# Kernel optimization log

Measured on AMD Instinct MI355X. Metric: run time of the kernel, lower is better.

## Reference

```python
import jax, jax.numpy as jnp
import numpy as np

EMB = 768
HEADS = 12


def setup_inputs() -> dict:
    key = jax.random.key(0)
    ks = jax.random.split(key, 5)
    B, N, E = 8, 1024, EMB
    x = jax.random.normal(ks[0], (B, N, E), dtype=jnp.float32)
    s = 1.0 / np.sqrt(E)
    W_qkv = jax.random.normal(ks[1], (E, 3 * E), dtype=jnp.float32) * s
    b_qkv = jnp.zeros((3 * E,), dtype=jnp.float32)
    W_fc = jax.random.normal(ks[2], (E, E), dtype=jnp.float32) * s
    b_fc = jnp.zeros((E,), dtype=jnp.float32)
    return {"x": x, "W_qkv": W_qkv, "b_qkv": b_qkv, "W_fc": W_fc, "b_fc": b_fc}


def reference(x, W_qkv, b_qkv, W_fc, b_fc):
    B, N, E = x.shape
    H = HEADS
    D = E // H
    qkv = x @ W_qkv + b_qkv                      # [B, N, 3E]
    q, k, v = jnp.split(qkv, 3, axis=-1)
    # b n (h d) -> b h n d
    def to_heads(t):
        return t.reshape(B, N, H, D).transpose(0, 2, 1, 3)
    q, k, v = to_heads(q), to_heads(k), to_heads(v)
    scale = 1.0 / jnp.sqrt(jnp.float32(E))       # NOTE: scales by sqrt(emb_size), not head dim
    attn = jnp.einsum('bhid,bhjd->bhij', q, k) * scale
    attn = jax.nn.softmax(attn, axis=-1)
    out = jnp.einsum('bhij,bhjd->bhid', attn, v)
    out = out.transpose(0, 2, 1, 3).reshape(B, N, E)  # b h n d -> b n (h d)
    return out @ W_fc + b_fc
```

## Files before the change

### kernel.cpp

```cpp
#include <hip/hip_runtime.h>
#include <hip/hip_bf16.h>


typedef unsigned short u16;
typedef unsigned int u32;
typedef __attribute__((ext_vector_type(8))) short short8;
typedef __attribute__((ext_vector_type(4))) float f32x4;

#define DEV static __device__ __forceinline__

DEV u16 f2bf(float f) {
  union { float f; u32 u; } v; v.f = f;
  return (u16)((v.u + 0x7FFFu + ((v.u >> 16) & 1u)) >> 16);
}

DEV u32 pk2(float lo, float hi) {
  union { __hip_bfloat162 h2; u32 u; } v;
  v.h2.x = __float2bfloat16(lo);
  v.h2.y = __float2bfloat16(hi);
  return v.u;
}

DEV void gload_lds16(const void* g, void* l) {
  __builtin_amdgcn_global_load_lds(
      (const __attribute__((address_space(1))) void*)g,
      (__attribute__((address_space(3))) void*)l, 16, 0, 0);
}

__global__ void cvt_bf16_kernel(const float* __restrict__ in, u16* __restrict__ out, int n8) {
  int idx = blockIdx.x * blockDim.x + threadIdx.x;
  int stride = gridDim.x * blockDim.x;
  for (int i = idx; i < n8; i += stride) {
    float4 a = reinterpret_cast<const float4*>(in)[2 * i];
    float4 b = reinterpret_cast<const float4*>(in)[2 * i + 1];
    uint4 o;
    o.x = f2bf(a.x) | ((u32)f2bf(a.y) << 16);
    o.y = f2bf(a.z) | ((u32)f2bf(a.w) << 16);
    o.z = f2bf(b.x) | ((u32)f2bf(b.y) << 16);
    o.w = f2bf(b.z) | ((u32)f2bf(b.w) << 16);
    reinterpret_cast<uint4*>(out)[i] = o;
  }
}

__global__ void trcvt_kernel(const float* __restrict__ in, u16* __restrict__ out,
                             int K, int Nn) {
  __shared__ u16 tile[64][72];
  int ntiles = Nn >> 6;
  int tk = blockIdx.x / ntiles, tn = blockIdx.x % ntiles;
  int k0 = tk << 6, n0 = tn << 6;
  int t = threadIdx.x;
  int r = t >> 4;
  int c4 = (t & 15) << 2;
#pragma unroll
  for (int ps = 0; ps < 4; ++ps) {
    int k = r + ps * 16;
    float4 v = *reinterpret_cast<const float4*>(&in[(size_t)(k0 + k) * Nn + n0 + c4]);
    tile[c4 + 0][k] = f2bf(v.x);
    tile[c4 + 1][k] = f2bf(v.y);
    tile[c4 + 2][k] = f2bf(v.z);
    tile[c4 + 3][k] = f2bf(v.w);
  }
  __syncthreads();
  int nr = t >> 3;
  int c8 = (t & 7) << 3;
#pragma unroll
  for (int ps = 0; ps < 2; ++ps) {
    int n = nr + ps * 32;
    uint4 v = *reinterpret_cast<const uint4*>(&tile[n][c8]);
    *reinterpret_cast<uint4*>(&out[(size_t)(n0 + n) * K + k0 + c8]) = v;
  }
}

template <int MODE>
__global__ __launch_bounds__(256, 4) void gemm_bt(
    const u16* __restrict__ A, const u16* __restrict__ Bt,
    const float* __restrict__ bias, void* __restrict__ Cout,
    u16* __restrict__ qh, u16* __restrict__ kh, u16* __restrict__ vt,
    int Nn) {
  __shared__ u16 As[2][128 * 32];
  __shared__ u16 Bs[2][128 * 32];
  const int nTn = Nn >> 7;
  const int nwg = gridDim.x;
  int wg = blockIdx.x;
  wg = (wg & 7) * (nwg >> 3) + (wg >> 3);
  const int tm = wg / nTn, tn = wg % nTn;
  const int m0 = tm << 7, n0 = tn << 7;
  const int tid = threadIdx.x;
  const int w = tid >> 6, lane = tid & 63;
  const int g = lane >> 4, p = lane & 15;
  const int wr = w >> 1, wc = w & 1;

  const int srow = lane >> 2;
  const int schunk = (lane & 3) ^ ((srow >> 1) & 3);
  const u16* Asrc = A + (size_t)(m0 + srow) * 768 + schunk * 8;
  const u16* Bsrc = Bt + (size_t)(n0 + srow) * 768 + schunk * 8;
  const int csw = (g ^ ((p >> 1) & 3)) << 3;

  f32x4 acc[4][4] = {};

#define STAGE(kt, sbuf)                                                         \
  do {                                                                          \
    _Pragma("unroll")                                                           \
    for (int i = 0; i < 2; ++i) {                                               \
      int trow = w * 32 + i * 16;                                               \
      gload_lds16(Asrc + (size_t)trow * 768 + (kt) * 32, &As[sbuf][trow * 32]); \
      gload_lds16(Bsrc + (size_t)trow * 768 + (kt) * 32, &Bs[sbuf][trow * 32]); \
    }                                                                           \
  } while (0)

  STAGE(0, 0);
  __syncthreads();

  int buf = 0;
  for (int k = 0; k < 24; ++k) {
    const u16* as = As[buf];
    const u16* bs = Bs[buf];
    short8 af[4], bf[4];
#pragma unroll
    for (int mb = 0; mb < 4; ++mb)
      af[mb] = *reinterpret_cast<const short8*>(&as[(wr * 64 + mb * 16 + p) * 32 + csw]);
#pragma unroll
    for (int nb = 0; nb < 4; ++nb)
      bf[nb] = *reinterpret_cast<const short8*>(&bs[(wc * 64 + nb * 16 + p) * 32 + csw]);
    if (k < 23) STAGE(k + 1, buf ^ 1);
#pragma unroll
    for (int mb = 0; mb < 4; ++mb)
#pragma unroll
      for (int nb = 0; nb < 4; ++nb)
        acc[mb][nb] = __builtin_amdgcn_mfma_f32_16x16x32_bf16(af[mb], bf[nb], acc[mb][nb], 0, 0, 0);
    __syncthreads();
    buf ^= 1;
  }
#undef STAGE

  const float qscale = 0.05205878290161879f;
#pragma unroll
  for (int nb = 0; nb < 4; ++nb) {
    int ncol = n0 + wc * 64 + nb * 16 + p;
    float bv = bias[ncol];
    if (MODE == 0) {
#pragma unroll
      for (int mb = 0; mb < 4; ++mb)
#pragma unroll
        for (int r = 0; r < 4; ++r) {
          int m = m0 + wr * 64 + mb * 16 + g * 4 + r;
          ((float*)Cout)[(size_t)m * Nn + ncol] = acc[mb][nb][r] + bv;
        }
    } else {
      int h64 = ncol >> 6;
      int which = h64 / 12;
      int hh = h64 - which * 12;
      int d = ncol & 63;
#pragma unroll
      for (int mb = 0; mb < 4; ++mb)
#pragma unroll
        for (int r = 0; r < 4; ++r) {
          int m = m0 + wr * 64 + mb * 16 + g * 4 + r;
          int bb = m >> 10, nr = m & 1023;
          float vv = acc[mb][nb][r] + bv;
          if (which == 2) {
            vt[((size_t)(bb * 12 + hh) * 64 + d) * 1024 + nr] = f2bf(vv);
          } else {
            u16* dst = which == 0 ? qh : kh;
            float sc = which == 0 ? qscale : 1.f;
            dst[(((size_t)bb * 12 + hh) * 1024 + nr) * 64 + d] = f2bf(vv * sc);
          }
        }
    }
  }
}

__global__ __launch_bounds__(512, 6) void attn_kernel(
    const u16* __restrict__ qh, const u16* __restrict__ kh,
    const u16* __restrict__ vt, u16* __restrict__ ao) {
  __shared__ u16 Ks[2][64 * 64];
  __shared__ u16 Vs[2][64 * 64];
  __shared__ u16 Ps[8][16 * 64];
  const int bid = blockIdx.x;
  const int qt = bid & 7;
  const int bh = bid >> 3;
  const int b = bh / 12, h = bh % 12;
  const int tid = threadIdx.x;
  const int w = tid >> 6, lane = tid & 63;
  const int g = lane >> 4, p = lane & 15;
  const int qrow = qt * 128 + w * 16;

  const u16* qbase = qh + ((size_t)bh * 1024 + qrow + p) * 64;
  short8 qf0 = *reinterpret_cast<const short8*>(qbase + g * 8);
  short8 qf1 = *reinterpret_cast<const short8*>(qbase + 32 + g * 8);

  const int ci = w * 64 + lane;
  const int crow = ci >> 3;
  const int csw = (ci & 7) ^ (crow & 7);
  const u16* ksrc = kh + (((size_t)bh * 1024 + crow) << 6) + csw * 8;
  const u16* vsrc = vt + ((size_t)bh * 64 + crow) * 1024 + csw * 8;
  u16* myp = Ps[w];

  const int sw = p & 7;
  const int c0 = (g ^ sw) << 3;
  const int c1 = ((4 + g) ^ sw) << 3;

  float m_run = -1e30f, l_run = 0.f;
  f32x4 oacc[4] = {};

  gload_lds16(ksrc, &Ks[0][w * 512]);
  gload_lds16(vsrc, &Vs[0][w * 512]);
  __syncthreads();

  int buf = 0;
  for (int kt = 0; kt < 1024; kt += 64) {
    if (kt < 960) {
      gload_lds16(ksrc + ((kt + 64) << 6), &Ks[buf ^ 1][w * 512]);
      gload_lds16(vsrc + (kt + 64), &Vs[buf ^ 1][w * 512]);
    }

    f32x4 s[4];
    __builtin_amdgcn_s_setprio(1);
#pragma unroll
    for (int jb = 0; jb < 4; ++jb) {
      const u16* kb = &Ks[buf][(jb * 16 + p) * 64];
      short8 k0 = *reinterpret_cast<const short8*>(kb + c0);
      short8 k1 = *reinterpret_cast<const short8*>(kb + c1);
      f32x4 z = {};
      z = __builtin_amdgcn_mfma_f32_16x16x32_bf16(k0, qf0, z, 0, 0, 0);
      z = __builtin_amdgcn_mfma_f32_16x16x32_bf16(k1, qf1, z, 0, 0, 0);
      s[jb] = z;
    }
    __builtin_amdgcn_s_setprio(0);

    float tmax = -1e30f;
#pragma unroll
    for (int jb = 0; jb < 4; ++jb)
#pragma unroll
      for (int r = 0; r < 4; ++r) tmax = fmaxf(tmax, s[jb][r]);
    tmax = fmaxf(tmax, __shfl_xor(tmax, 16));
    tmax = fmaxf(tmax, __shfl_xor(tmax, 32));

    if (!__all(tmax - m_run <= 8.f)) {
      float m_new = fmaxf(m_run, tmax);
      float alpha = __builtin_amdgcn_exp2f(m_run - m_new);
      float al[4];
#pragma unroll
      for (int r = 0; r < 4; ++r) al[r] = __shfl(alpha, g * 4 + r);
#pragma unroll
      for (int nb = 0; nb < 4; ++nb)
#pragma unroll
        for (int r = 0; r < 4; ++r) oacc[nb][r] *= al[r];
      l_run *= alpha;
      m_run = m_new;
    }

    float lsum = 0.f;
#pragma unroll
    for (int jb = 0; jb < 4; ++jb)
#pragma unroll
      for (int r = 0; r < 4; ++r) {
        float e = __builtin_amdgcn_exp2f(s[jb][r] - m_run);
        s[jb][r] = e;
        lsum += e;
      }
    lsum += __shfl_xor(lsum, 16);
    lsum += __shfl_xor(lsum, 32);
    l_run += lsum;

#pragma unroll
    for (int jb = 0; jb < 4; ++jb) {
      uint2 pkv;
      pkv.x = pk2(s[jb][0], s[jb][1]);
      pkv.y = pk2(s[jb][2], s[jb][3]);
      int c = 2 * jb + (g >> 1);
      *reinterpret_cast<uint2*>(&myp[p * 64 + ((c ^ sw) << 3) + ((g & 1) << 2)]) = pkv;
    }

    short8 pa0 = *reinterpret_cast<const short8*>(&myp[p * 64 + c0]);
    short8 pa1 = *reinterpret_cast<const short8*>(&myp[p * 64 + c1]);
    __builtin_amdgcn_s_setprio(1);
#pragma unroll
    for (int nb = 0; nb < 4; ++nb) {
      const u16* vb = &Vs[buf][(nb * 16 + p) * 64];
      short8 v0 = *reinterpret_cast<const short8*>(vb + c0);
      short8 v1 = *reinterpret_cast<const short8*>(vb + c1);
      oacc[nb] = __builtin_amdgcn_mfma_f32_16x16x32_bf16(pa0, v0, oacc[nb], 0, 0, 0);
      oacc[nb] = __builtin_amdgcn_mfma_f32_16x16x32_bf16(pa1, v1, oacc[nb], 0, 0, 0);
    }
    __builtin_amdgcn_s_setprio(0);

    __syncthreads();
    buf ^= 1;
  }

  float li[4];
#pragma unroll
  for (int r = 0; r < 4; ++r) li[r] = 1.f / __shfl(l_run, g * 4 + r);
  u16* obase = ao + ((size_t)(b * 1024 + qrow)) * 768 + h * 64;
#pragma unroll
  for (int nb = 0; nb < 4; ++nb)
#pragma unroll
    for (int r = 0; r < 4; ++r)
      obase[(size_t)(g * 4 + r) * 768 + nb * 16 + p] = f2bf(oacc[nb][r] * li[r]);
}

extern "C" void kernel_launch(void* const* d_in, const int* in_sizes, int n_in,
                              void* d_out, int out_size, void* d_ws, size_t ws_size,
                              hipStream_t stream) {
  const float* x = (const float*)d_in[0];
  const float* Wqkv = (const float*)d_in[1];
  const float* bqkv = (const float*)d_in[2];
  const float* Wfc = (const float*)d_in[3];
  const float* bfc = (const float*)d_in[4];
  float* out = (float*)d_out;

  char* ws = (char*)d_ws;
  u16* xb    = (u16*)(ws);
  u16* wqkvT = (u16*)(ws + 12582912);
  u16* wfcT  = (u16*)(ws + 16121856);
  u16* qh    = (u16*)(ws + 17301504);
  u16* kh    = (u16*)(ws + 29884416);
  u16* vt    = (u16*)(ws + 55050240);
  u16* ao    = (u16*)(ws + 67633152);

  cvt_bf16_kernel<<<2048, 256, 0, stream>>>(x, xb, (8192 * 768) / 8);
  trcvt_kernel<<<12 * 36, 256, 0, stream>>>(Wqkv, wqkvT, 768, 2304);
  trcvt_kernel<<<12 * 12, 256, 0, stream>>>(Wfc, wfcT, 768, 768);
  gemm_bt<2><<<64 * 18, 256, 0, stream>>>(xb, wqkvT, bqkv, nullptr, qh, kh, vt, 2304);
  attn_kernel<<<96 * 8, 512, 0, stream>>>(qh, kh, vt, ao);
  gemm_bt<0><<<64 * 6, 256, 0, stream>>>(ao, wfcT, bfc, out, nullptr, nullptr, nullptr, 768);
}
```

Before: 142.7 us.

## Fuse prep conversions into one kernel and stage V transpose through LDS

Result: faster. 124.1 us, median of 2 (-13.1%).

```diff
diff --git a/kernel.cpp b/kernel.cpp
--- a/kernel.cpp
+++ b/kernel.cpp
@@ -27,47 +27,56 @@
       (__attribute__((address_space(3))) void*)l, 16, 0, 0);
 }
 
-__global__ void cvt_bf16_kernel(const float* __restrict__ in, u16* __restrict__ out, int n8) {
-  int idx = blockIdx.x * blockDim.x + threadIdx.x;
-  int stride = gridDim.x * blockDim.x;
-  for (int i = idx; i < n8; i += stride) {
-    float4 a = reinterpret_cast<const float4*>(in)[2 * i];
-    float4 b = reinterpret_cast<const float4*>(in)[2 * i + 1];
-    uint4 o;
-    o.x = f2bf(a.x) | ((u32)f2bf(a.y) << 16);
-    o.y = f2bf(a.z) | ((u32)f2bf(a.w) << 16);
-    o.z = f2bf(b.x) | ((u32)f2bf(b.y) << 16);
-    o.w = f2bf(b.z) | ((u32)f2bf(b.w) << 16);
-    reinterpret_cast<uint4*>(out)[i] = o;
-  }
-}
-
-__global__ void trcvt_kernel(const float* __restrict__ in, u16* __restrict__ out,
-                             int K, int Nn) {
+__global__ void prep_kernel(const float* __restrict__ x, u16* __restrict__ xb,
+                            const float* __restrict__ Wq, u16* __restrict__ WqT,
+                            const float* __restrict__ Wf, u16* __restrict__ WfT) {
   __shared__ u16 tile[64][72];
-  int ntiles = Nn >> 6;
-  int tk = blockIdx.x / ntiles, tn = blockIdx.x % ntiles;
-  int k0 = tk << 6, n0 = tn << 6;
-  int t = threadIdx.x;
-  int r = t >> 4;
-  int c4 = (t & 15) << 2;
-#pragma unroll
-  for (int ps = 0; ps < 4; ++ps) {
-    int k = r + ps * 16;
-    float4 v = *reinterpret_cast<const float4*>(&in[(size_t)(k0 + k) * Nn + n0 + c4]);
-    tile[c4 + 0][k] = f2bf(v.x);
-    tile[c4 + 1][k] = f2bf(v.y);
-    tile[c4 + 2][k] = f2bf(v.z);
-    tile[c4 + 3][k] = f2bf(v.w);
-  }
-  __syncthreads();
-  int nr = t >> 3;
-  int c8 = (t & 7) << 3;
-#pragma unroll
-  for (int ps = 0; ps < 2; ++ps) {
-    int n = nr + ps * 32;
-    uint4 v = *reinterpret_cast<const uint4*>(&tile[n][c8]);
-    *reinterpret_cast<uint4*>(&out[(size_t)(n0 + n) * K + k0 + c8]) = v;
+  const int b = blockIdx.x;
+  const int t = threadIdx.x;
+  if (b < 576) {
+    const float* in;
+    u16* out;
+    int Nn, bid;
+    if (b < 432) { in = Wq; out = WqT; Nn = 2304; bid = b; }
+    else         { in = Wf; out = WfT; Nn = 768;  bid = b - 432; }
+    const int K = 768;
+    int ntiles = Nn >> 6;
+    int tk = bid / ntiles, tn = bid % ntiles;
+    int k0 = tk << 6, n0 = tn << 6;
+    int r = t >> 4;
+    int c4 = (t & 15) << 2;
+#pragma unroll
+    for (int ps = 0; ps < 4; ++ps) {
+      int k = r + ps * 16;
+      float4 v = *reinterpret_cast<const float4*>(&in[(size_t)(k0 + k) * Nn + n0 + c4]);
+      tile[c4 + 0][k] = f2bf(v.x);
+      tile[c4 + 1][k] = f2bf(v.y);
+      tile[c4 + 2][k] = f2bf(v.z);
+      tile[c4 + 3][k] = f2bf(v.w);
+    }
+    __syncthreads();
+    int nr = t >> 3;
+    int c8 = (t & 7) << 3;
+#pragma unroll
+    for (int ps = 0; ps < 2; ++ps) {
+      int n = nr + ps * 32;
+      uint4 v = *reinterpret_cast<const uint4*>(&tile[n][c8]);
+      *reinterpret_cast<uint4*>(&out[(size_t)(n0 + n) * K + k0 + c8]) = v;
+    }
+  } else {
+    const int n8 = (8192 * 768) / 8;
+    int idx = (b - 576) * 256 + t;
+    const int stride = 2048 * 256;
+    for (int i = idx; i < n8; i += stride) {
+      float4 a = reinterpret_cast<const float4*>(x)[2 * i];
+      float4 c = reinterpret_cast<const float4*>(x)[2 * i + 1];
+      uint4 o;
+      o.x = f2bf(a.x) | ((u32)f2bf(a.y) << 16);
+      o.y = f2bf(a.z) | ((u32)f2bf(a.w) << 16);
+      o.z = f2bf(c.x) | ((u32)f2bf(c.y) << 16);
+      o.w = f2bf(c.z) | ((u32)f2bf(c.w) << 16);
+      reinterpret_cast<uint4*>(xb)[i] = o;
+    }
   }
 }
 
@@ -77,8 +86,11 @@
     const float* __restrict__ bias, void* __restrict__ Cout,
     u16* __restrict__ qh, u16* __restrict__ kh, u16* __restrict__ vt,
     int Nn) {
-  __shared__ u16 As[2][128 * 32];
-  __shared__ u16 Bs[2][128 * 32];
+  __shared__ u16 SMEM[17408];
+  u16* const As0 = SMEM;
+  u16* const As1 = SMEM + 4096;
+  u16* const Bs0 = SMEM + 8192;
+  u16* const Bs1 = SMEM + 12288;
   const int nTn = Nn >> 7;
   const int nwg = gridDim.x;
   int wg = blockIdx.x;
@@ -98,23 +110,23 @@
 
   f32x4 acc[4][4] = {};
 
-#define STAGE(kt, sbuf)                                                         \
+#define STAGE(kt, ap, bp)                                                       \
   do {                                                                          \
     _Pragma("unroll")                                                           \
     for (int i = 0; i < 2; ++i) {                                               \
       int trow = w * 32 + i * 16;                                               \
-      gload_lds16(Asrc + (size_t)trow * 768 + (kt) * 32, &As[sbuf][trow * 32]); \
-      gload_lds16(Bsrc + (size_t)trow * 768 + (kt) * 32, &Bs[sbuf][trow * 32]); \
+      gload_lds16(Asrc + (size_t)trow * 768 + (kt) * 32, (ap) + trow * 32);     \
+      gload_lds16(Bsrc + (size_t)trow * 768 + (kt) * 32, (bp) + trow * 32);     \
     }                                                                           \
   } while (0)
 
-  STAGE(0, 0);
+  STAGE(0, As0, Bs0);
   __syncthreads();
 
   int buf = 0;
   for (int k = 0; k < 24; ++k) {
-    const u16* as = As[buf];
-    const u16* bs = Bs[buf];
+    const u16* as = buf ? As1 : As0;
+    const u16* bs = buf ? Bs1 : Bs0;
     short8 af[4], bf[4];
 #pragma unroll
     for (int mb = 0; mb < 4; ++mb)
@@ -122,7 +134,7 @@
 #pragma unroll
     for (int nb = 0; nb < 4; ++nb)
       bf[nb] = *reinterpret_cast<const short8*>(&bs[(wc * 64 + nb * 16 + p) * 32 + csw]);
-    if (k < 23) STAGE(k + 1, buf ^ 1);
+    if (k < 23) STAGE(k + 1, buf ? As0 : As1, buf ? Bs0 : Bs1);
 #pragma unroll
     for (int mb = 0; mb < 4; ++mb)
 #pragma unroll
@@ -134,11 +146,11 @@
 #undef STAGE
 
   const float qscale = 0.05205878290161879f;
-#pragma unroll
-  for (int nb = 0; nb < 4; ++nb) {
-    int ncol = n0 + wc * 64 + nb * 16 + p;
-    float bv = bias[ncol];
-    if (MODE == 0) {
+  if (MODE == 0) {
+#pragma unroll
+    for (int nb = 0; nb < 4; ++nb) {
+      int ncol = n0 + wc * 64 + nb * 16 + p;
+      float bv = bias[ncol];
 #pragma unroll
       for (int mb = 0; mb < 4; ++mb)
 #pragma unroll
@@ -146,26 +158,56 @@
           int m = m0 + wr * 64 + mb * 16 + g * 4 + r;
           ((float*)Cout)[(size_t)m * Nn + ncol] = acc[mb][nb][r] + bv;
         }
-    } else {
+    }
+  } else if (n0 < 1536) {
+#pragma unroll
+    for (int nb = 0; nb < 4; ++nb) {
+      int ncol = n0 + wc * 64 + nb * 16 + p;
+      float bv = bias[ncol];
       int h64 = ncol >> 6;
       int which = h64 / 12;
       int hh = h64 - which * 12;
       int d = ncol & 63;
+      u16* dst = which == 0 ? qh : kh;
+      float sc = which == 0 ? qscale : 1.f;
 #pragma unroll
       for (int mb = 0; mb < 4; ++mb)
 #pragma unroll
         for (int r = 0; r < 4; ++r) {
           int m = m0 + wr * 64 + mb * 16 + g * 4 + r;
           int bb = m >> 10, nr = m & 1023;
-          float vv = acc[mb][nb][r] + bv;
-          if (which == 2) {
-            vt[((size_t)(bb * 12 + hh) * 64 + d) * 1024 + nr] = f2bf(vv);
-          } else {
-            u16* dst = which == 0 ? qh : kh;
-            float sc = which == 0 ? qscale : 1.f;
-            dst[(((size_t)bb * 12 + hh) * 1024 + nr) * 64 + d] = f2bf(vv * sc);
-          }
+          dst[(((size_t)bb * 12 + hh) * 1024 + nr) * 64 + d] = f2bf((acc[mb][nb][r] + bv) * sc);
         }
+    }
+  } else {
+#pragma unroll
+    for (int nb = 0; nb < 4; ++nb) {
+      int nl = wc * 64 + nb * 16 + p;
+      float bv = bias[n0 + nl];
+#pragma unroll
+      for (int mb = 0; mb < 4; ++mb) {
+        int mlb = wr * 64 + mb * 16 + g * 4;
+        uint2 pkv;
+        pkv.x = (u32)f2bf(acc[mb][nb][0] + bv) | ((u32)f2bf(acc[mb][nb][1] + bv) << 16);
+        pkv.y = (u32)f2bf(acc[mb][nb][2] + bv) | ((u32)f2bf(acc[mb][nb][3] + bv) << 16);
+        *reinterpret_cast<uint2*>(&SMEM[nl * 136 + mlb]) = pkv;
+      }
+    }
+    __syncthreads();
+    const int hhb = (n0 - 1536) >> 6;
+    const int bb = m0 >> 10;
+    const int nseq0 = m0 & 1023;
+    const int c16 = (tid & 7) * 16;
+#pragma unroll
+    for (int ps = 0; ps < 4; ++ps) {
+      int nl = (tid >> 3) + ps * 32;
+      int hh = hhb + (nl >> 6);
+      int d = nl & 63;
+      u16* dst = vt + (((size_t)(bb * 12 + hh) * 64 + d) << 10) + nseq0 + c16;
+      uint4 v0 = *reinterpret_cast<const uint4*>(&SMEM[nl * 136 + c16]);
+      uint4 v1 = *reinterpret_cast<const uint4*>(&SMEM[nl * 136 + c16 + 8]);
+      *reinterpret_cast<uint4*>(dst) = v0;
+      *reinterpret_cast<uint4*>(dst + 8) = v1;
     }
   }
 }
@@ -319,9 +361,7 @@
   u16* vt    = (u16*)(ws + 55050240);
   u16* ao    = (u16*)(ws + 67633152);
 
-  cvt_bf16_kernel<<<2048, 256, 0, stream>>>(x, xb, (8192 * 768) / 8);
-  trcvt_kernel<<<12 * 36, 256, 0, stream>>>(Wqkv, wqkvT, 768, 2304);
-  trcvt_kernel<<<12 * 12, 256, 0, stream>>>(Wfc, wfcT, 768, 768);
+  prep_kernel<<<2624, 256, 0, stream>>>(x, xb, Wqkv, wqkvT, Wfc, wfcT);
   gemm_bt<2><<<64 * 18, 256, 0, stream>>>(xb, wqkvT, bqkv, nullptr, qh, kh, vt, 2304);
   attn_kernel<<<96 * 8, 512, 0, stream>>>(qh, kh, vt, ao);
   gemm_bt<0><<<64 * 6, 256, 0, stream>>>(ao, wfcT, bfc, out, nullptr, nullptr, nullptr, 768);
```
